# Performance work log

Measured on AMD Instinct MI355X. Metric: run time of the kernel, lower is better.

The kernel has to match this reference:

```python
import jax, jax.numpy as jnp
import numpy as np

N_HEADS, D_K, D_MODEL = 16, 64, 1024
B, S = 2, 2048


def setup_inputs() -> dict:
    key = jax.random.key(0)
    ks = jax.random.split(key, 9)
    scale = 1.0 / np.sqrt(D_MODEL)
    cscale = 1.0 / np.sqrt(N_HEADS * D_K)
    return {
        "x": jax.random.normal(ks[0], (B, S, D_MODEL), dtype=jnp.float32),
        # per-head projection weights, stacked over heads: [H, d_model, d_k]
        "Wq": jax.random.uniform(ks[1], (N_HEADS, D_MODEL, D_K), jnp.float32, -scale, scale),
        "bq": jax.random.uniform(ks[2], (N_HEADS, D_K), jnp.float32, -scale, scale),
        "Wk": jax.random.uniform(ks[3], (N_HEADS, D_MODEL, D_K), jnp.float32, -scale, scale),
        "bk": jax.random.uniform(ks[4], (N_HEADS, D_K), jnp.float32, -scale, scale),
        "Wv": jax.random.uniform(ks[5], (N_HEADS, D_MODEL, D_K), jnp.float32, -scale, scale),
        "bv": jax.random.uniform(ks[6], (N_HEADS, D_K), jnp.float32, -scale, scale),
        # concat projection: [H*d_k, d_model]
        "Wc": jax.random.uniform(ks[7], (N_HEADS * D_K, D_MODEL), jnp.float32, -cscale, cscale),
        "bc": jax.random.uniform(ks[8], (D_MODEL,), jnp.float32, -cscale, cscale),
    }


def reference(x, Wq, bq, Wk, bk, Wv, bv, Wc, bc):
    # Per-head projections, vectorized across heads: [B,H,S,d_k]
    q = jnp.einsum("bsd,hdk->bhsk", x, Wq) + bq[None, :, None, :]
    k = jnp.einsum("bsd,hdk->bhsk", x, Wk) + bk[None, :, None, :]
    v = jnp.einsum("bsd,hdk->bhsk", x, Wv) + bv[None, :, None, :]
    # scores: [B,H,Sq,Skv]
    scores = jnp.einsum("bhsk,bhtk->bhst", q, k) / jnp.sqrt(jnp.asarray(D_K, x.dtype))
    # FAITHFUL to original: softmax over dim=1 of [B,S,S] = the QUERY axis (axis 2 here)
    attn = jax.nn.softmax(scores, axis=2)
    out = jnp.einsum("bhst,bhtk->bhsk", attn, v)  # [B,H,S,d_k]
    # concat heads along feature dim: [B,S,H*d_k]
    cat = jnp.transpose(out, (0, 2, 1, 3)).reshape(x.shape[0], x.shape[1], -1)
    return cat @ Wc + bc
```

## Files before the change

kernel.cpp:

```cpp
#include <hip/hip_runtime.h>
#include <hip/hip_bf16.h>

#define NH 16
#define DK 64
#define DM 1024
#define BB 2
#define SS 2048
#define BS (BB*SS)

typedef __attribute__((ext_vector_type(8))) short bf16x8;
typedef __attribute__((ext_vector_type(4))) short short4v;
typedef __attribute__((ext_vector_type(4))) float f32x4;

#define MFMA16 __builtin_amdgcn_mfma_f32_16x16x32_bf16

static __device__ __forceinline__ float bf2f(short s) {
  union { unsigned u; float f; } v;
  v.u = ((unsigned)(unsigned short)s) << 16;
  return v.f;
}
static __device__ __forceinline__ short f2bf(float f) {
  union { float f; unsigned u; } v; v.f = f;
  unsigned r = (v.u + 0x7fffu + ((v.u >> 16) & 1u)) >> 16;
  return (short)r;
}
static __device__ __forceinline__ unsigned pkbf(float a, float b) {
  __hip_bfloat162 h = __float22bfloat162_rn(make_float2(a, b));
  union { __hip_bfloat162 h; unsigned u; } c; c.h = h; return c.u;
}

template<int C16>
static __device__ __forceinline__ int soff(int row, int chunk) {
  return row*(C16*8) + ((chunk ^ (row & (C16-1))) << 3);
}

template<int C16, int R>
static __device__ __forceinline__ void stage(const short* __restrict__ g, int gstride,
                                             short* l, int wave, int lane) {
  const int rloc = lane / C16;
  const int c    = lane % C16;
#pragma unroll
  for (int rr = 0; rr < R; rr += 4*(64/C16)) {
    int rbase = rr + wave*(64/C16);
    int row   = rbase + rloc;
    int cg    = c ^ (row & (C16-1));
    __builtin_amdgcn_global_load_lds(
        (const __attribute__((address_space(1))) void*)(g + (size_t)row*gstride + cg*8),
        (__attribute__((address_space(3))) void*)(l + rbase*(C16*8)),
        16, 0, 0);
  }
}

__global__ __launch_bounds__(256) void k_convert(
    const float* __restrict__ x,
    const float* __restrict__ Wq, const float* __restrict__ Wk,
    const float* __restrict__ Wv, const float* __restrict__ Wc,
    short* __restrict__ xb, short* __restrict__ Wt, short* __restrict__ Wct) {
  __shared__ float T[64][65];
  const int tid = threadIdx.x;
  int bx = blockIdx.x;
  const int XB = BS*DM/(256*4);
  if (bx < XB) {
    int i = (bx*256 + tid)*4;
    float4 v = *(const float4*)&x[i];
    union { unsigned u[2]; short4v s; } o;
    o.u[0] = pkbf(v.x, v.y); o.u[1] = pkbf(v.z, v.w);
    *(short4v*)&xb[i] = o.s;
    return;
  }
  bx -= XB;
  if (bx < 48*16) {
    int th = bx >> 4, d0 = (bx & 15) * 64;
    int type = th >> 4, h = th & 15;
    const float* W = ((type == 0) ? Wq : (type == 1) ? Wk : Wv)
                     + (size_t)h*DM*DK + (size_t)d0*DK;
#pragma unroll
    for (int p = 0; p < 4; p++) {
      int dr = p*16 + (tid >> 4), dkc = (tid & 15) * 4;
      float4 v = *(const float4*)&W[(size_t)dr*DK + dkc];
      T[dkc+0][dr]=v.x; T[dkc+1][dr]=v.y; T[dkc+2][dr]=v.z; T[dkc+3][dr]=v.w;
    }
    __syncthreads();
#pragma unroll
    for (int e = 0; e < 2; e++) {
      int c = tid*2 + e, dk = c >> 3, dd = (c & 7) * 8;
      union { short s[8]; int4 v; } u;
#pragma unroll
      for (int j = 0; j < 8; j++) u.s[j] = f2bf(T[dk][dd+j]);
      *(int4*)&Wt[((size_t)th*DK + dk)*DM + d0 + dd] = u.v;
    }
    return;
  }
  bx -= 48*16;
  int n0 = (bx >> 4) * 64, k0 = (bx & 15) * 64;
#pragma unroll
  for (int p = 0; p < 4; p++) {
    int kr = p*16 + (tid >> 4), nc = (tid & 15) * 4;
    float4 v = *(const float4*)&Wc[(size_t)(k0+kr)*DM + n0 + nc];
    T[nc+0][kr]=v.x; T[nc+1][kr]=v.y; T[nc+2][kr]=v.z; T[nc+3][kr]=v.w;
  }
  __syncthreads();
#pragma unroll
  for (int e = 0; e < 2; e++) {
    int c = tid*2 + e, n = c >> 3, kk = (c & 7) * 8;
    union { short s[8]; int4 v; } u;
#pragma unroll
    for (int j = 0; j < 8; j++) u.s[j] = f2bf(T[n][kk+j]);
    *(int4*)&Wct[(size_t)(n0+n)*DM + k0 + kk] = u.v;
  }
}

__global__ __launch_bounds__(256) void k_qkv(
    const short* __restrict__ xb, const short* __restrict__ Wt,
    const float* __restrict__ bq, const float* __restrict__ bk,
    const float* __restrict__ bv,
    short* __restrict__ Qb, short* __restrict__ Kb, short* __restrict__ Vb) {
  __shared__ __align__(16) short As[128*64];
  __shared__ __align__(16) short Bs[128*64];
  const int tid = threadIdx.x, wave = tid >> 6, lane = tid & 63;
  const int l15 = lane & 15, quad = lane >> 4;
  const int id = blockIdx.x, xcd = id & 7, j = id >> 3;
  const int m0 = (xcd*4 + (j & 3)) * 128, n0 = (j >> 2) * 128;
  const int mw = (wave & 1) * 64, nw = (wave >> 1) * 64;
  f32x4 acc[4][4] = {};
  for (int k0 = 0; k0 < DM; k0 += 64) {
    stage<8,128>(xb + (size_t)m0*DM + k0, DM, As, wave, lane);
    stage<8,128>(Wt + (size_t)n0*DM + k0, DM, Bs, wave, lane);
    __syncthreads();
#pragma unroll
    for (int ks = 0; ks < 2; ks++) {
      bf16x8 a[4], b[4];
#pragma unroll
      for (int g = 0; g < 4; g++)  a[g]  = *(const bf16x8*)&As[soff<8>(mw + g*16 + l15,  ks*4 + quad)];
#pragma unroll
      for (int nf = 0; nf < 4; nf++) b[nf] = *(const bf16x8*)&Bs[soff<8>(nw + nf*16 + l15, ks*4 + quad)];
#pragma unroll
      for (int g = 0; g < 4; g++)
#pragma unroll
        for (int nf = 0; nf < 4; nf++)
          acc[g][nf] = MFMA16(a[g], b[nf], acc[g][nf], 0, 0, 0);
    }
    __syncthreads();
  }
  const int th = (n0 + nw) >> 6;
  const int type = th >> 4, h = th & 15;
  short* dst = (type == 0) ? Qb : (type == 1) ? Kb : Vb;
  const float* bias = ((type == 0) ? bq : (type == 1) ? bk : bv) + h*DK;
  const float scale = (type == 0) ? 0.125f : 1.0f;
#pragma unroll
  for (int nf = 0; nf < 4; nf++) {
    int dk = nf*16 + l15;
    float bval = bias[dk];
#pragma unroll
    for (int g = 0; g < 4; g++)
#pragma unroll
      for (int r = 0; r < 4; r++) {
        int m = m0 + mw + g*16 + quad*4 + r;
        int b_ = m >> 11, s = m & (SS-1);
        dst[(size_t)((b_*NH + h)*SS + s)*DK + dk] = f2bf((acc[g][nf][r] + bval) * scale);
      }
  }
}

__global__ __launch_bounds__(256) void k_stats(
    const short* __restrict__ Qb, const short* __restrict__ Kb,
    const short* __restrict__ Vb, short* __restrict__ Vt) {
  __shared__ __align__(16) short smem[3*8192];
  __shared__ float red[4][64];
  __shared__ float zinv[128];
  short* Ks = smem;
  const int tid = threadIdx.x, wave = tid >> 6, lane = tid & 63;
  const int l15 = lane & 15, quad = lane >> 4;
  const int id = blockIdx.x, xcd = id & 7, j = id >> 3;
  const int bh = xcd*4 + (j & 3), t0 = (j >> 2) * 128;
  const short* Qg = Qb + (size_t)bh * SS * DK;
  const short* Kg = Kb + (size_t)bh * SS * DK;
  const int mw = (wave & 1) * 64, nw = (wave >> 1) * 64;
  stage<8,128>(Kg + (size_t)t0*DK, DK, Ks, wave, lane);
  stage<8,128>(Qg, DK, smem + 8192, wave, lane);
  __syncthreads();
  bf16x8 kf[2][4];
#pragma unroll
  for (int ks = 0; ks < 2; ks++)
#pragma unroll
    for (int nf = 0; nf < 4; nf++)
      kf[ks][nf] = *(const bf16x8*)&Ks[soff<8>(nw + nf*16 + l15, ks*4 + quad)];
  float csum[4] = {0.f, 0.f, 0.f, 0.f};
  for (int it = 0; it < SS/128; it++) {
    if (it + 1 < SS/128)
      stage<8,128>(Qg + (size_t)(it+1)*128*DK, DK,
                   smem + 8192 + (((it+1) & 1) << 13), wave, lane);
    const short* Qs = smem + 8192 + ((it & 1) << 13);
    f32x4 acc[4][4] = {};
#pragma unroll
    for (int ks = 0; ks < 2; ks++) {
      bf16x8 a[4];
#pragma unroll
      for (int g = 0; g < 4; g++) a[g] = *(const bf16x8*)&Qs[soff<8>(mw + g*16 + l15, ks*4 + quad)];
#pragma unroll
      for (int g = 0; g < 4; g++)
#pragma unroll
        for (int nf = 0; nf < 4; nf++)
          acc[g][nf] = MFMA16(a[g], kf[ks][nf], acc[g][nf], 0, 0, 0);
    }
#pragma unroll
    for (int nf = 0; nf < 4; nf++)
#pragma unroll
      for (int g = 0; g < 4; g++)
#pragma unroll
        for (int r = 0; r < 4; r++)
          csum[nf] += __expf(acc[g][nf][r]);
    __syncthreads();
  }
#pragma unroll
  for (int nf = 0; nf < 4; nf++) {
    csum[nf] += __shfl_xor(csum[nf], 16, 64);
    csum[nf] += __shfl_xor(csum[nf], 32, 64);
  }
  if (lane < 16) {
#pragma unroll
    for (int nf = 0; nf < 4; nf++) red[wave][nf*16 + lane] = csum[nf];
  }
  __syncthreads();
  if (tid < 128) {
    int half = tid >> 6, c = tid & 63;
    zinv[tid] = 1.0f / (red[half*2][c] + red[half*2 + 1][c]);
  }
  __syncthreads();
  short* Vtile = smem + 8192;
  const short* Vg = Vb + (size_t)bh * SS * DK;
#pragma unroll
  for (int it = 0; it < 4; it++) {
    int c = tid + it*256;
    int trow = c >> 3, c8 = (c & 7) * 8;
    union { int4 v; short s[8]; } u;
    u.v = *(const int4*)&Vg[(size_t)(t0 + trow)*DK + c8];
    float sc = zinv[trow];
#pragma unroll
    for (int jj = 0; jj < 8; jj++) {
      int dk = c8 + jj;
      Vtile[dk*128 + (((trow >> 3) ^ (dk & 15)) << 3) + (trow & 7)] = f2bf(bf2f(u.s[jj]) * sc);
    }
  }
  __syncthreads();
  short* Vtg = Vt + (size_t)bh * DK * SS;
#pragma unroll
  for (int it = 0; it < 4; it++) {
    int row = it*16 + (tid >> 4), cc = tid & 15;
    *(int4*)&Vtg[(size_t)row*SS + t0 + cc*8] = *(const int4*)&Vtile[soff<16>(row, cc)];
  }
}

__global__ __launch_bounds__(256, 2) void k_attnpv(
    const short* __restrict__ Qb, const short* __restrict__ Kb,
    const short* __restrict__ Vt, short* __restrict__ catg) {
  __shared__ __align__(16) short smem[40960];
  short* Qs = smem;
  short* Ps = smem;
  short* Ks = smem + 16384;
  const int tid = threadIdx.x, wave = tid >> 6, lane = tid & 63;
  const int l15 = lane & 15, quad = lane >> 4;
  const int id = blockIdx.x, xcd = id & 7, jj = id >> 3;
  const int bh = xcd*4 + (jj & 3), s0 = (jj >> 2) * 128;
  const int b = bh >> 4, h = bh & 15;
  const short* Qg  = Qb + (size_t)bh * SS * DK;
  const short* Kg  = Kb + (size_t)bh * SS * DK;
  const short* Vtg = Vt + (size_t)bh * DK * SS;
  const int th_ = wave & 1, sh = wave >> 1;
  stage<8,128>(Qg + (size_t)s0*DK, DK, Qs, wave, lane);
  stage<8,128>(Kg, DK, Ks, wave, lane);
  stage<16,64>(Vtg, SS, smem + 24576, wave, lane);
  __syncthreads();
  bf16x8 qf[2][4];
#pragma unroll
  for (int ks = 0; ks < 2; ks++)
#pragma unroll
    for (int nf = 0; nf < 4; nf++)
      qf[ks][nf] = *(const bf16x8*)&Qs[soff<8>(sh*64 + nf*16 + l15, ks*4 + quad)];
  __syncthreads();
  f32x4 out[4][4] = {};
  for (int it = 0; it < SS/128; it++) {
    f32x4 sacc[4][4] = {};
#pragma unroll
    for (int ks = 0; ks < 2; ks++) {
      bf16x8 a[4];
#pragma unroll
      for (int g = 0; g < 4; g++)
        a[g] = *(const bf16x8*)&Ks[soff<8>(th_*64 + g*16 + l15, ks*4 + quad)];
#pragma unroll
      for (int g = 0; g < 4; g++)
#pragma unroll
        for (int nf = 0; nf < 4; nf++)
          sacc[g][nf] = MFMA16(a[g], qf[ks][nf], sacc[g][nf], 0, 0, 0);
    }
#pragma unroll
    for (int g = 0; g < 4; g++)
#pragma unroll
      for (int nf = 0; nf < 4; nf++) {
        int s_loc = sh*64 + nf*16 + l15;
        int ct = th_*8 + g*2 + (quad >> 1);
        uint2 p;
        p.x = pkbf(__expf(sacc[g][nf][0]), __expf(sacc[g][nf][1]));
        p.y = pkbf(__expf(sacc[g][nf][2]), __expf(sacc[g][nf][3]));
        *(uint2*)&Ps[s_loc*128 + ((ct ^ (s_loc & 15)) << 3) + ((quad & 1) << 2)] = p;
      }
    __syncthreads();
    if (it + 1 < SS/128) {
      stage<8,128>(Kg + (size_t)(it+1)*128*DK, DK, Ks, wave, lane);
      stage<16,64>(Vtg + (it+1)*128, SS, smem + 24576 + (((it+1) & 1) << 13), wave, lane);
    }
    const short* Vs = smem + 24576 + ((it & 1) << 13);
#pragma unroll
    for (int ks = 0; ks < 2; ks++) {
      bf16x8 pa[4], vb[4];
#pragma unroll
      for (int g = 0; g < 4; g++) {
        int s_loc = sh*64 + g*16 + l15;
        int ct2 = th_*8 + ks*4 + quad;
        pa[g] = *(const bf16x8*)&Ps[s_loc*128 + ((ct2 ^ (s_loc & 15)) << 3)];
      }
#pragma unroll
      for (int nf = 0; nf < 4; nf++)
        vb[nf] = *(const bf16x8*)&Vs[soff<16>(nf*16 + l15, th_*8 + ks*4 + quad)];
#pragma unroll
      for (int g = 0; g < 4; g++)
#pragma unroll
        for (int nf = 0; nf < 4; nf++)
          out[g][nf] = MFMA16(pa[g], vb[nf], out[g][nf], 0, 0, 0);
    }
    __syncthreads();
  }
  float* Pf = (float*)smem;
  if (th_) {
#pragma unroll
    for (int g = 0; g < 4; g++)
#pragma unroll
      for (int nf = 0; nf < 4; nf++)
#pragma unroll
        for (int r = 0; r < 4; r++)
          Pf[sh*4096 + (g*16 + quad*4 + r)*64 + nf*16 + l15] = out[g][nf][r];
  }
  __syncthreads();
  if (!th_) {
#pragma unroll
    for (int g = 0; g < 4; g++)
#pragma unroll
      for (int nf = 0; nf < 4; nf++)
#pragma unroll
        for (int r = 0; r < 4; r++) {
          float v = out[g][nf][r] + Pf[sh*4096 + (g*16 + quad*4 + r)*64 + nf*16 + l15];
          int s = s0 + sh*64 + g*16 + quad*4 + r;
          catg[(size_t)(b*SS + s)*DM + h*DK + nf*16 + l15] = f2bf(v);
        }
  }
}

__global__ __launch_bounds__(256) void k_final(
    const short* __restrict__ catg, const short* __restrict__ Wct,
    const float* __restrict__ bc, float* __restrict__ out) {
  __shared__ __align__(16) short As[128*64];
  __shared__ __align__(16) short Bs[128*64];
  const int tid = threadIdx.x, wave = tid >> 6, lane = tid & 63;
  const int l15 = lane & 15, quad = lane >> 4;
  const int id = blockIdx.x, xcd = id & 7, j = id >> 3;
  const int m0 = (xcd*4 + (j & 3)) * 128, n0 = (j >> 2) * 128;
  const int mw = (wave & 1) * 64, nw = (wave >> 1) * 64;
  f32x4 acc[4][4] = {};
  for (int k0 = 0; k0 < DM; k0 += 64) {
    stage<8,128>(catg + (size_t)m0*DM + k0, DM, As, wave, lane);
    stage<8,128>(Wct  + (size_t)n0*DM + k0, DM, Bs, wave, lane);
    __syncthreads();
#pragma unroll
    for (int ks = 0; ks < 2; ks++) {
      bf16x8 a[4], b[4];
#pragma unroll
      for (int g = 0; g < 4; g++)  a[g]  = *(const bf16x8*)&As[soff<8>(mw + g*16 + l15,  ks*4 + quad)];
#pragma unroll
      for (int nf = 0; nf < 4; nf++) b[nf] = *(const bf16x8*)&Bs[soff<8>(nw + nf*16 + l15, ks*4 + quad)];
#pragma unroll
      for (int g = 0; g < 4; g++)
#pragma unroll
        for (int nf = 0; nf < 4; nf++)
          acc[g][nf] = MFMA16(a[g], b[nf], acc[g][nf], 0, 0, 0);
    }
    __syncthreads();
  }
#pragma unroll
  for (int nf = 0; nf < 4; nf++) {
    int n = n0 + nw + nf*16 + l15;
    float bval = bc[n];
#pragma unroll
    for (int g = 0; g < 4; g++)
#pragma unroll
      for (int r = 0; r < 4; r++) {
        int m = m0 + mw + g*16 + quad*4 + r;
        out[(size_t)m*DM + n] = acc[g][nf][r] + bval;
      }
  }
}

extern "C" void kernel_launch(void* const* d_in, const int* in_sizes, int n_in,
                              void* d_out, int out_size, void* d_ws, size_t ws_size,
                              hipStream_t stream) {
  (void)in_sizes; (void)n_in; (void)out_size; (void)ws_size;
  const float* x  = (const float*)d_in[0];
  const float* Wq = (const float*)d_in[1];
  const float* bq = (const float*)d_in[2];
  const float* Wk = (const float*)d_in[3];
  const float* bk = (const float*)d_in[4];
  const float* Wv = (const float*)d_in[5];
  const float* bv = (const float*)d_in[6];
  const float* Wc = (const float*)d_in[7];
  const float* bc = (const float*)d_in[8];
  float* out = (float*)d_out;

  char* ws = (char*)d_ws;
  size_t o = 0;
  short* xb  = (short*)(ws + o); o += (size_t)BS*DM*2;
  short* Wt  = (short*)(ws + o); o += (size_t)3*NH*DK*DM*2;
  short* Wct = (short*)(ws + o); o += (size_t)DM*DM*2;
  short* Qb  = (short*)(ws + o); o += (size_t)BB*NH*SS*DK*2;
  short* Kb  = (short*)(ws + o); o += (size_t)BB*NH*SS*DK*2;
  short* Vb  = (short*)(ws + o); o += (size_t)BB*NH*SS*DK*2;
  short* Vt  = (short*)(ws + o); o += (size_t)BB*NH*DK*SS*2;
  short* cat = (short*)(ws + o); o += (size_t)BS*DM*2;

  const int nconv = BS*DM/(256*4) + 48*16 + 256;
  k_convert<<<dim3(nconv), 256, 0, stream>>>(x, Wq, Wk, Wv, Wc, xb, Wt, Wct);
  k_qkv   <<<dim3(768), 256, 0, stream>>>(xb, Wt, bq, bk, bv, Qb, Kb, Vb);
  k_stats <<<dim3(512), 256, 0, stream>>>(Qb, Kb, Vb, Vt);
  k_attnpv<<<dim3(512), 256, 0, stream>>>(Qb, Kb, Vt, cat);
  k_final <<<dim3(256), 256, 0, stream>>>(cat, Wct, bc, out);
}
```

Before: 225.7 us.

## Keep P in registers for PV MFMA, double-buffer K, use exp2 with prescaled Q

The attention kernel no longer writes the exponentiated scores to LDS and reads them back. The score accumulator layout is fed straight into 16x16x16 bf16 MFMAs as the A operand, which removes one barrier and the P shared-memory round trip per tile. K is now double-buffered like V, and shared memory drops to 64KB. Q is prescaled by log2(e)/8 so the kernels can use native exp2 instead of expf. The cost is that the K16 MFMA variant needs twice as many instructions for the PV product, and the V operand now takes narrower 8-byte LDS reads.

```diff
diff --git a/kernel.cpp b/kernel.cpp
--- a/kernel.cpp
+++ b/kernel.cpp
@@ -13,6 +13,21 @@
 typedef __attribute__((ext_vector_type(4))) float f32x4;
 
 #define MFMA16 __builtin_amdgcn_mfma_f32_16x16x32_bf16
+
+static __device__ __forceinline__ f32x4 MFMA16K16(short4v a, short4v b, f32x4 c) {
+#if __has_builtin(__builtin_amdgcn_mfma_f32_16x16x16bf16_1k)
+  return __builtin_amdgcn_mfma_f32_16x16x16bf16_1k(a, b, c, 0, 0, 0);
+#else
+  asm volatile("v_mfma_f32_16x16x16_bf16 %0, %1, %2, %0" : "+v"(c) : "v"(a), "v"(b));
+  return c;
+#endif
+}
+
+#if __has_builtin(__builtin_amdgcn_exp2f)
+#define EXP2(x) __builtin_amdgcn_exp2f(x)
+#else
+#define EXP2(x) __expf((x) * 0.6931471805599453f)
+#endif
 
 static __device__ __forceinline__ float bf2f(short s) {
   union { unsigned u; float f; } v;
@@ -146,7 +161,7 @@
   const int type = th >> 4, h = th & 15;
   short* dst = (type == 0) ? Qb : (type == 1) ? Kb : Vb;
   const float* bias = ((type == 0) ? bq : (type == 1) ? bk : bv) + h*DK;
-  const float scale = (type == 0) ? 0.125f : 1.0f;
+  const float scale = (type == 0) ? 0.18033688011112042f : 1.0f;
 #pragma unroll
   for (int nf = 0; nf < 4; nf++) {
     int dk = nf*16 + l15;
@@ -209,7 +224,7 @@
       for (int g = 0; g < 4; g++)
 #pragma unroll
         for (int r = 0; r < 4; r++)
-          csum[nf] += __expf(acc[g][nf][r]);
+          csum[nf] += EXP2(acc[g][nf][r]);
     __syncthreads();
   }
 #pragma unroll
@@ -254,10 +269,7 @@
 __global__ __launch_bounds__(256, 2) void k_attnpv(
     const short* __restrict__ Qb, const short* __restrict__ Kb,
     const short* __restrict__ Vt, short* __restrict__ catg) {
-  __shared__ __align__(16) short smem[40960];
-  short* Qs = smem;
-  short* Ps = smem;
-  short* Ks = smem + 16384;
+  __shared__ __align__(16) short smem[32768];
   const int tid = threadIdx.x, wave = tid >> 6, lane = tid & 63;
   const int l15 = lane & 15, quad = lane >> 4;
   const int id = blockIdx.x, xcd = id & 7, jj = id >> 3;
@@ -267,19 +279,21 @@
   const short* Kg  = Kb + (size_t)bh * SS * DK;
   const short* Vtg = Vt + (size_t)bh * DK * SS;
   const int th_ = wave & 1, sh = wave >> 1;
-  stage<8,128>(Qg + (size_t)s0*DK, DK, Qs, wave, lane);
-  stage<8,128>(Kg, DK, Ks, wave, lane);
-  stage<16,64>(Vtg, SS, smem + 24576, wave, lane);
+  stage<8,128>(Qg + (size_t)s0*DK, DK, smem + 8192, wave, lane);
+  stage<8,128>(Kg, DK, smem, wave, lane);
+  stage<16,64>(Vtg, SS, smem + 16384, wave, lane);
   __syncthreads();
   bf16x8 qf[2][4];
 #pragma unroll
   for (int ks = 0; ks < 2; ks++)
 #pragma unroll
     for (int nf = 0; nf < 4; nf++)
-      qf[ks][nf] = *(const bf16x8*)&Qs[soff<8>(sh*64 + nf*16 + l15, ks*4 + quad)];
+      qf[ks][nf] = *(const bf16x8*)&smem[8192 + soff<8>(sh*64 + nf*16 + l15, ks*4 + quad)];
   __syncthreads();
   f32x4 out[4][4] = {};
   for (int it = 0; it < SS/128; it++) {
+    const short* Ks = smem + ((it & 1) << 13);
+    const short* Vs = smem + 16384 + ((it & 1) << 13);
     f32x4 sacc[4][4] = {};
 #pragma unroll
     for (int ks = 0; ks < 2; ks++) {
@@ -293,64 +307,58 @@
         for (int nf = 0; nf < 4; nf++)
           sacc[g][nf] = MFMA16(a[g], qf[ks][nf], sacc[g][nf], 0, 0, 0);
     }
+    short4v pa[4][4];
 #pragma unroll
     for (int g = 0; g < 4; g++)
 #pragma unroll
       for (int nf = 0; nf < 4; nf++) {
-        int s_loc = sh*64 + nf*16 + l15;
-        int ct = th_*8 + g*2 + (quad >> 1);
-        uint2 p;
-        p.x = pkbf(__expf(sacc[g][nf][0]), __expf(sacc[g][nf][1]));
-        p.y = pkbf(__expf(sacc[g][nf][2]), __expf(sacc[g][nf][3]));
-        *(uint2*)&Ps[s_loc*128 + ((ct ^ (s_loc & 15)) << 3) + ((quad & 1) << 2)] = p;
+        union { unsigned u[2]; short4v s; } pu;
+        pu.u[0] = pkbf(EXP2(sacc[g][nf][0]), EXP2(sacc[g][nf][1]));
+        pu.u[1] = pkbf(EXP2(sacc[g][nf][2]), EXP2(sacc[g][nf][3]));
+        pa[nf][g] = pu.s;
       }
-    __syncthreads();
     if (it + 1 < SS/128) {
-      stage<8,128>(Kg + (size_t)(it+1)*128*DK, DK, Ks, wave, lane);
-      stage<16,64>(Vtg + (it+1)*128, SS, smem + 24576 + (((it+1) & 1) << 13), wave, lane);
-    }
-    const short* Vs = smem + 24576 + ((it & 1) << 13);
-#pragma unroll
-    for (int ks = 0; ks < 2; ks++) {
-      bf16x8 pa[4], vb[4];
-#pragma unroll
-      for (int g = 0; g < 4; g++) {
-        int s_loc = sh*64 + g*16 + l15;
-        int ct2 = th_*8 + ks*4 + quad;
-        pa[g] = *(const bf16x8*)&Ps[s_loc*128 + ((ct2 ^ (s_loc & 15)) << 3)];
+      stage<8,128>(Kg + (size_t)(it+1)*128*DK, DK, smem + (((it+1) & 1) << 13), wave, lane);
+      stage<16,64>(Vtg + (it+1)*128, SS, smem + 16384 + (((it+1) & 1) << 13), wave, lane);
+    }
+#pragma unroll
+    for (int g = 0; g < 4; g++) {
+      short4v vb[4];
+#pragma unroll
+      for (int nv = 0; nv < 4; nv++) {
+        int row = nv*16 + l15;
+        int ct = (8*th_ + 2*g + (quad >> 1)) ^ (row & 15);
+        vb[nv] = *(const short4v*)&Vs[row*128 + (ct << 3) + ((quad & 1) << 2)];
       }
 #pragma unroll
       for (int nf = 0; nf < 4; nf++)
-        vb[nf] = *(const bf16x8*)&Vs[soff<16>(nf*16 + l15, th_*8 + ks*4 + quad)];
-#pragma unroll
-      for (int g = 0; g < 4; g++)
-#pragma unroll
-        for (int nf = 0; nf < 4; nf++)
-          out[g][nf] = MFMA16(pa[g], vb[nf], out[g][nf], 0, 0, 0);
+#pragma unroll
+        for (int nv = 0; nv < 4; nv++)
+          out[nf][nv] = MFMA16K16(pa[nf][g], vb[nv], out[nf][nv]);
     }
     __syncthreads();
   }
   float* Pf = (float*)smem;
   if (th_) {
 #pragma unroll
-    for (int g = 0; g < 4; g++)
-#pragma unroll
-      for (int nf = 0; nf < 4; nf++)
+    for (int nf = 0; nf < 4; nf++)
+#pragma unroll
+      for (int nv = 0; nv < 4; nv++)
 #pragma unroll
         for (int r = 0; r < 4; r++)
-          Pf[sh*4096 + (g*16 + quad*4 + r)*64 + nf*16 + l15] = out[g][nf][r];
+          Pf[sh*4096 + (nf*16 + quad*4 + r)*64 + nv*16 + l15] = out[nf][nv][r];
   }
   __syncthreads();
   if (!th_) {
 #pragma unroll
-    for (int g = 0; g < 4; g++)
-#pragma unroll
-      for (int nf = 0; nf < 4; nf++)
+    for (int nf = 0; nf < 4; nf++)
+#pragma unroll
+      for (int nv = 0; nv < 4; nv++)
 #pragma unroll
         for (int r = 0; r < 4; r++) {
-          float v = out[g][nf][r] + Pf[sh*4096 + (g*16 + quad*4 + r)*64 + nf*16 + l15];
-          int s = s0 + sh*64 + g*16 + quad*4 + r;
-          catg[(size_t)(b*SS + s)*DM + h*DK + nf*16 + l15] = f2bf(v);
+          float v = out[nf][nv][r] + Pf[sh*4096 + (nf*16 + quad*4 + r)*64 + nv*16 + l15];
+          int s = s0 + sh*64 + nf*16 + quad*4 + r;
+          catg[(size_t)(b*SS + s)*DM + h*DK + nv*16 + l15] = f2bf(v);
         }
   }
 }
```

Result: faster. 220.1 us (-2.5%).
